# Kernel optimization log

Measured on AMD Instinct MI355X. Metric: run time of the kernel, lower is better.

The kernel has to match this reference:

```python
import jax, jax.numpy as jnp
import numpy as np

SEQ = 64      # len(features): number of timesteps for the (seq-major) LSTM
B = 40        # the expand(.., 40, ..) axis -> LSTM batch dim (batch_first=False)
IN = 8192 * 2 # 16384
H = 1024


def setup_inputs() -> dict:
    key = jax.random.key(0)
    k1, k2, k3, k4, k5 = jax.random.split(key, 5)
    s = 1.0 / np.sqrt(H)  # PyTorch LSTM init scale
    features = jax.random.normal(k1, (SEQ, IN), dtype=jnp.float32)
    w_ih = jax.random.uniform(k2, (4 * H, IN), jnp.float32, -s, s)
    w_hh = jax.random.uniform(k3, (4 * H, H), jnp.float32, -s, s)
    b_ih = jax.random.uniform(k4, (4 * H,), jnp.float32, -s, s)
    b_hh = jax.random.uniform(k5, (4 * H,), jnp.float32, -s, s)
    return {"features": features, "w_ih": w_ih, "w_hh": w_hh, "b_ih": b_ih, "b_hh": b_hh}


def reference(features, w_ih, w_hh, b_ih, b_hh):
    # features: [SEQ, IN]. The torch code expands each row to 40 identical
    # batch elements; since the input projection is identical across those
    # copies we compute it once per timestep and broadcast over B.
    xw = features @ w_ih.T + (b_ih + b_hh)  # [SEQ, 4H], hoisted big GEMM

    def step(carry, xw_t):
        h, c = carry                      # each [B, H]
        gates = xw_t[None, :] + h @ w_hh.T  # [B, 4H]
        i, f, g, o = jnp.split(gates, 4, axis=-1)  # PyTorch gate order i,f,g,o
        i = jax.nn.sigmoid(i)
        f = jax.nn.sigmoid(f)
        g = jnp.tanh(g)
        o = jax.nn.sigmoid(o)
        c = f * c + i * g
        h = o * jnp.tanh(c)
        return (h, c), h

    h0 = jnp.zeros((B, H), dtype=features.dtype)
    c0 = jnp.zeros((B, H), dtype=features.dtype)
    _, hs = jax.lax.scan(step, (h0, c0), xw)
    return hs  # [SEQ, B, H] == (seq_len, batch, hidden) as torch returns
```

## Files before the change

kernel.cpp:

```cpp
#include <hip/hip_runtime.h>
#include <hip/hip_bf16.h>
#include <math.h>

#define SEQ 64
#define IN_DIM 16384
#define H_DIM 1024
#define G4 4096
#define BATCH 40
#define NB_SCAN 64
#define NT_SCAN 1024

#define OFF_FT   256
#define OFF_XW   (OFF_FT + (size_t)IN_DIM*SEQ)
#define OFF_H    (OFF_XW + (size_t)SEQ*G4)
#define OFF_HS   (OFF_H + H_DIM)
#define OFF_PART (OFF_HS + (size_t)SEQ*H_DIM)

__global__ void zero_bar(unsigned* bar) {
    bar[threadIdx.x] = 0u;
}

__global__ __launch_bounds__(256) void transpose_f(const float* __restrict__ f,
                                                   float* __restrict__ fT) {
    __shared__ float lds[64][65];
    const int kb = blockIdx.x;
    const int tx = threadIdx.x & 63;
    const int ty = threadIdx.x >> 6;
#pragma unroll
    for (int i = 0; i < 16; ++i) {
        int t = ty * 16 + i;
        lds[tx][t] = f[(size_t)t * IN_DIM + kb * 64 + tx];
    }
    __syncthreads();
#pragma unroll
    for (int i = 0; i < 16; ++i) {
        int r = ty * 16 + i;
        fT[(size_t)(kb * 64 + r) * 64 + tx] = lds[r][tx];
    }
}

__global__ __launch_bounds__(256) void gemm_partial(const float* __restrict__ w_ih,
                                                    const float* __restrict__ fT,
                                                    float* __restrict__ part,
                                                    int kspan) {
    const int tid = threadIdx.x;
    const int j  = blockIdx.x * 256 + tid;
    const int t0 = blockIdx.y * 16;
    const int k0 = blockIdx.z * kspan;

    float acc[16];
#pragma unroll
    for (int i = 0; i < 16; ++i) acc[i] = 0.f;

    const float* wrow = w_ih + (size_t)j * IN_DIM;
    for (int kc = k0; kc < k0 + kspan; kc += 16) {
        const float4* wp = (const float4*)(wrow + kc);
        float warr[16];
        *(float4*)&warr[0]  = wp[0];
        *(float4*)&warr[4]  = wp[1];
        *(float4*)&warr[8]  = wp[2];
        *(float4*)&warr[12] = wp[3];
        const float* fbase = fT + (size_t)kc * 64 + t0;
#pragma unroll
        for (int kk = 0; kk < 16; ++kk) {
            const float wv = warr[kk];
            const float4* fp = (const float4*)(fbase + kk * 64);
            float4 f0 = fp[0], f1 = fp[1], f2 = fp[2], f3 = fp[3];
            acc[0]  += wv * f0.x; acc[1]  += wv * f0.y; acc[2]  += wv * f0.z; acc[3]  += wv * f0.w;
            acc[4]  += wv * f1.x; acc[5]  += wv * f1.y; acc[6]  += wv * f1.z; acc[7]  += wv * f1.w;
            acc[8]  += wv * f2.x; acc[9]  += wv * f2.y; acc[10] += wv * f2.z; acc[11] += wv * f2.w;
            acc[12] += wv * f3.x; acc[13] += wv * f3.y; acc[14] += wv * f3.z; acc[15] += wv * f3.w;
        }
    }
    float* pp = part + ((size_t)blockIdx.z * SEQ + t0) * G4 + j;
#pragma unroll
    for (int i = 0; i < 16; ++i) pp[(size_t)i * G4] = acc[i];
}

__global__ __launch_bounds__(256) void reduce_xw(const float* __restrict__ part,
                                                 const float* __restrict__ b_ih,
                                                 const float* __restrict__ b_hh,
                                                 float* __restrict__ xw, int KS) {
    const int idx = blockIdx.x * 256 + threadIdx.x;
    const int j = idx & (G4 - 1);
    float s = b_ih[j] + b_hh[j];
    for (int ks = 0; ks < KS; ++ks) s += part[(size_t)ks * (SEQ * G4) + idx];
    xw[idx] = s;
}

__global__ __launch_bounds__(NT_SCAN, 1) void lstm_scan(const float* __restrict__ xw,
                                                        const float* __restrict__ w_hh,
                                                        float* __restrict__ h_buf,
                                                        float* __restrict__ hs_c,
                                                        unsigned* __restrict__ bar) {
    const int tid = threadIdx.x;
    const int b = blockIdx.x;
    const int r  = tid & 63;
    const int q  = tid >> 6;
    const int g  = r >> 4;
    const int jl = r & 15;
    const size_t grow = (size_t)g * H_DIM + (size_t)b * 16 + jl;

    float4 w[16];
    {
        const float4* wp = (const float4*)(w_hh + grow * H_DIM + q * 64);
#pragma unroll
        for (int m = 0; m < 16; ++m) w[m] = wp[m];
    }
#pragma unroll
    for (int m = 0; m < 16; ++m) {
        asm volatile("" : "+v"(w[m].x), "+v"(w[m].y), "+v"(w[m].z), "+v"(w[m].w));
    }

    __shared__ float h_lds[H_DIM];
    __shared__ float red[64][17];
    __shared__ float gate_lds[64];

    float c_reg = 0.f;

    for (int t = 0; t < SEQ; ++t) {
        float part = 0.f;
        if (t > 0) {
            h_lds[tid] = __hip_atomic_load(h_buf + tid, __ATOMIC_RELAXED,
                                           __HIP_MEMORY_SCOPE_AGENT);
            __syncthreads();
#pragma unroll
            for (int m = 0; m < 16; ++m) {
                float4 h4 = *(const float4*)&h_lds[q * 64 + m * 4];
                part += w[m].x * h4.x + w[m].y * h4.y + w[m].z * h4.z + w[m].w * h4.w;
            }
        }
        red[r][q] = part;
        __syncthreads();
        if (tid < 64) {
            float s = 0.f;
#pragma unroll
            for (int qq = 0; qq < 16; ++qq) s += red[tid][qq];
            const int gg = tid >> 4;
            const int jj = b * 16 + (tid & 15);
            gate_lds[tid] = xw[(size_t)t * G4 + (size_t)gg * H_DIM + jj] + s;
        }
        __syncthreads();
        if (tid < 16) {
            float iv = gate_lds[tid];
            float fv = gate_lds[16 + tid];
            float gv = gate_lds[32 + tid];
            float ov = gate_lds[48 + tid];
            iv = 1.f / (1.f + expf(-iv));
            fv = 1.f / (1.f + expf(-fv));
            gv = tanhf(gv);
            ov = 1.f / (1.f + expf(-ov));
            c_reg = fv * c_reg + iv * gv;
            float hv = ov * tanhf(c_reg);
            const int j = b * 16 + tid;
            hs_c[(size_t)t * H_DIM + j] = hv;
            __hip_atomic_store(h_buf + j, hv, __ATOMIC_RELAXED,
                               __HIP_MEMORY_SCOPE_AGENT);
        }
        if (t < SEQ - 1) {
            __syncthreads();
            asm volatile("s_waitcnt vmcnt(0)" ::: "memory");
            if (tid == 0) {
                __hip_atomic_fetch_add(bar, 1u, __ATOMIC_RELAXED, __HIP_MEMORY_SCOPE_AGENT);
                const unsigned target = (unsigned)(NB_SCAN * (t + 1));
                while (__hip_atomic_load(bar, __ATOMIC_RELAXED, __HIP_MEMORY_SCOPE_AGENT) < target) {
                    __builtin_amdgcn_s_sleep(1);
                }
                asm volatile("" ::: "memory");
            }
            __syncthreads();
        }
    }
}

__global__ __launch_bounds__(256) void bcast_out(const float* __restrict__ hs_c,
                                                 float* __restrict__ out) {
    const int gi = blockIdx.x * 256 + threadIdx.x;
    const int t = gi / (BATCH * (H_DIM / 4));
    const int rem = gi - t * (BATCH * (H_DIM / 4));
    const int jq = rem & (H_DIM / 4 - 1);
    const float4 v = ((const float4*)hs_c)[t * (H_DIM / 4) + jq];
    ((float4*)out)[gi] = v;
}

extern "C" void kernel_launch(void* const* d_in, const int* in_sizes, int n_in,
                              void* d_out, int out_size, void* d_ws, size_t ws_size,
                              hipStream_t stream) {
    const float* features = (const float*)d_in[0];
    const float* w_ih     = (const float*)d_in[1];
    const float* w_hh     = (const float*)d_in[2];
    const float* b_ih     = (const float*)d_in[3];
    const float* b_hh     = (const float*)d_in[4];
    float* out = (float*)d_out;
    float* ws  = (float*)d_ws;

    float* fT    = ws + OFF_FT;
    float* xw    = ws + OFF_XW;
    float* h_buf = ws + OFF_H;
    float* hs_c  = ws + OFF_HS;
    float* part  = ws + OFF_PART;
    unsigned* bar = (unsigned*)d_ws;

    int KS = 16;
    while (KS > 1 && (OFF_PART + (size_t)KS * SEQ * G4) * 4 > ws_size) KS >>= 1;
    const int kspan = IN_DIM / KS;

    zero_bar<<<1, 256, 0, stream>>>(bar);
    transpose_f<<<IN_DIM / 64, 256, 0, stream>>>(features, fT);
    gemm_partial<<<dim3(G4 / 256, SEQ / 16, KS), 256, 0, stream>>>(w_ih, fT, part, kspan);
    reduce_xw<<<(SEQ * G4) / 256, 256, 0, stream>>>(part, b_ih, b_hh, xw, KS);
    lstm_scan<<<NB_SCAN, NT_SCAN, 0, stream>>>(xw, w_hh, h_buf, hs_c, bar);
    bcast_out<<<(SEQ * BATCH * H_DIM / 4) / 256, 256, 0, stream>>>(hs_c, out);
}
```

Baseline: 725.9 us.

## Use split-bf16 MFMA for input GEMM and per-block flag barrier in LSTM scan

Replaces the scalar FP32 input-projection GEMM with a bf16 MFMA kernel that splits both operands into hi/lo bf16 parts and uses three MFMAs to approximate FP32 precision. The feature transpose is replaced by a hi/lo conversion kernel, and the K-split count drops from 16 to 8. The LSTM scan drops the separate h buffer and reads h directly from the hs output, prefetches xw early in each step, and replaces the single atomic-counter barrier with per-block step flags polled by one wavefront. The split-bf16 approach drops the lo*lo term, adding a small precision loss, and weights are converted on the fly in every block.

```diff
diff --git a/kernel.cpp b/kernel.cpp
--- a/kernel.cpp
+++ b/kernel.cpp
@@ -10,71 +10,98 @@
 #define NB_SCAN 64
 #define NT_SCAN 1024
 
-#define OFF_FT   256
-#define OFF_XW   (OFF_FT + (size_t)IN_DIM*SEQ)
-#define OFF_H    (OFF_XW + (size_t)SEQ*G4)
-#define OFF_HS   (OFF_H + H_DIM)
-#define OFF_PART (OFF_HS + (size_t)SEQ*H_DIM)
-
-__global__ void zero_bar(unsigned* bar) {
-    bar[threadIdx.x] = 0u;
-}
-
-__global__ __launch_bounds__(256) void transpose_f(const float* __restrict__ f,
-                                                   float* __restrict__ fT) {
-    __shared__ float lds[64][65];
-    const int kb = blockIdx.x;
-    const int tx = threadIdx.x & 63;
-    const int ty = threadIdx.x >> 6;
-#pragma unroll
-    for (int i = 0; i < 16; ++i) {
-        int t = ty * 16 + i;
-        lds[tx][t] = f[(size_t)t * IN_DIM + kb * 64 + tx];
+typedef short bf16x8 __attribute__((ext_vector_type(8)));
+typedef float f32x4 __attribute__((ext_vector_type(4)));
+typedef unsigned int uvec4 __attribute__((ext_vector_type(4)));
+typedef unsigned int uvec2 __attribute__((ext_vector_type(2)));
+
+#define OFF_AH   256
+#define OFF_AL   (OFF_AH + (size_t)SEQ * IN_DIM / 2)
+#define OFF_XW   (OFF_AL + (size_t)SEQ * IN_DIM / 2)
+#define OFF_HS   (OFF_XW + (size_t)SEQ * G4)
+#define OFF_PART (OFF_HS + (size_t)SEQ * H_DIM)
+
+__global__ void zero_bar(unsigned* bar) { bar[threadIdx.x] = 0u; }
+
+__global__ __launch_bounds__(256) void convert_a(const float* __restrict__ f,
+                                                 unsigned* __restrict__ a_hi,
+                                                 unsigned* __restrict__ a_lo) {
+    const int i = blockIdx.x * 256 + threadIdx.x;
+    uvec4 u = ((const uvec4*)f)[i];
+    unsigned h0 = (u.x >> 16) | (u.y & 0xffff0000u);
+    unsigned h1 = (u.z >> 16) | (u.w & 0xffff0000u);
+    float l0 = __uint_as_float(u.x) - __uint_as_float(u.x & 0xffff0000u);
+    float l1 = __uint_as_float(u.y) - __uint_as_float(u.y & 0xffff0000u);
+    float l2 = __uint_as_float(u.z) - __uint_as_float(u.z & 0xffff0000u);
+    float l3 = __uint_as_float(u.w) - __uint_as_float(u.w & 0xffff0000u);
+    unsigned q0 = (__float_as_uint(l0) >> 16) | (__float_as_uint(l1) & 0xffff0000u);
+    unsigned q1 = (__float_as_uint(l2) >> 16) | (__float_as_uint(l3) & 0xffff0000u);
+    uvec2 hv; hv.x = h0; hv.y = h1;
+    uvec2 lv; lv.x = q0; lv.y = q1;
+    ((uvec2*)a_hi)[i] = hv;
+    ((uvec2*)a_lo)[i] = lv;
+}
+
+__global__ __launch_bounds__(256, 2) void gemm_mfma(const float* __restrict__ w_ih,
+                                                    const unsigned* __restrict__ a_hi,
+                                                    const unsigned* __restrict__ a_lo,
+                                                    float* __restrict__ part, int kspan) {
+    const int tid = threadIdx.x;
+    const int wv   = tid >> 6;
+    const int lane = tid & 63;
+    const int col  = lane & 15;
+    const int kg   = lane >> 4;
+    const int jbase = blockIdx.x * 64 + wv * 16 + col;
+    const int k0base = blockIdx.y * kspan;
+
+    const float* wrow = w_ih + (size_t)jbase * IN_DIM;
+
+    f32x4 acc[4] = {};
+
+    for (int k0 = k0base; k0 < k0base + kspan; k0 += 32) {
+        const int kf = k0 + kg * 8;
+        uvec4 u0 = *(const uvec4*)(wrow + kf);
+        uvec4 u1 = *(const uvec4*)(wrow + kf + 4);
+        uvec4 hb, lb;
+        hb.x = (u0.x >> 16) | (u0.y & 0xffff0000u);
+        hb.y = (u0.z >> 16) | (u0.w & 0xffff0000u);
+        hb.z = (u1.x >> 16) | (u1.y & 0xffff0000u);
+        hb.w = (u1.z >> 16) | (u1.w & 0xffff0000u);
+        float f0 = __uint_as_float(u0.x) - __uint_as_float(u0.x & 0xffff0000u);
+        float f1 = __uint_as_float(u0.y) - __uint_as_float(u0.y & 0xffff0000u);
+        float f2 = __uint_as_float(u0.z) - __uint_as_float(u0.z & 0xffff0000u);
+        float f3 = __uint_as_float(u0.w) - __uint_as_float(u0.w & 0xffff0000u);
+        float f4 = __uint_as_float(u1.x) - __uint_as_float(u1.x & 0xffff0000u);
+        float f5 = __uint_as_float(u1.y) - __uint_as_float(u1.y & 0xffff0000u);
+        float f6 = __uint_as_float(u1.z) - __uint_as_float(u1.z & 0xffff0000u);
+        float f7 = __uint_as_float(u1.w) - __uint_as_float(u1.w & 0xffff0000u);
+        lb.x = (__float_as_uint(f0) >> 16) | (__float_as_uint(f1) & 0xffff0000u);
+        lb.y = (__float_as_uint(f2) >> 16) | (__float_as_uint(f3) & 0xffff0000u);
+        lb.z = (__float_as_uint(f4) >> 16) | (__float_as_uint(f5) & 0xffff0000u);
+        lb.w = (__float_as_uint(f6) >> 16) | (__float_as_uint(f7) & 0xffff0000u);
+        bf16x8 bhi = __builtin_bit_cast(bf16x8, hb);
+        bf16x8 blo = __builtin_bit_cast(bf16x8, lb);
+
+#pragma unroll
+        for (int i = 0; i < 4; ++i) {
+            const size_t aidx = (size_t)(i * 16 + col) * (IN_DIM / 2) + (kf >> 1);
+            uvec4 ah = *(const uvec4*)(a_hi + aidx);
+            uvec4 al = *(const uvec4*)(a_lo + aidx);
+            bf16x8 ahv = __builtin_bit_cast(bf16x8, ah);
+            bf16x8 alv = __builtin_bit_cast(bf16x8, al);
+            acc[i] = __builtin_amdgcn_mfma_f32_16x16x32_bf16(ahv, bhi, acc[i], 0, 0, 0);
+            acc[i] = __builtin_amdgcn_mfma_f32_16x16x32_bf16(alv, bhi, acc[i], 0, 0, 0);
+            acc[i] = __builtin_amdgcn_mfma_f32_16x16x32_bf16(ahv, blo, acc[i], 0, 0, 0);
+        }
     }
-    __syncthreads();
-#pragma unroll
-    for (int i = 0; i < 16; ++i) {
-        int r = ty * 16 + i;
-        fT[(size_t)(kb * 64 + r) * 64 + tx] = lds[r][tx];
-    }
-}
-
-__global__ __launch_bounds__(256) void gemm_partial(const float* __restrict__ w_ih,
-                                                    const float* __restrict__ fT,
-                                                    float* __restrict__ part,
-                                                    int kspan) {
-    const int tid = threadIdx.x;
-    const int j  = blockIdx.x * 256 + tid;
-    const int t0 = blockIdx.y * 16;
-    const int k0 = blockIdx.z * kspan;
-
-    float acc[16];
-#pragma unroll
-    for (int i = 0; i < 16; ++i) acc[i] = 0.f;
-
-    const float* wrow = w_ih + (size_t)j * IN_DIM;
-    for (int kc = k0; kc < k0 + kspan; kc += 16) {
-        const float4* wp = (const float4*)(wrow + kc);
-        float warr[16];
-        *(float4*)&warr[0]  = wp[0];
-        *(float4*)&warr[4]  = wp[1];
-        *(float4*)&warr[8]  = wp[2];
-        *(float4*)&warr[12] = wp[3];
-        const float* fbase = fT + (size_t)kc * 64 + t0;
-#pragma unroll
-        for (int kk = 0; kk < 16; ++kk) {
-            const float wv = warr[kk];
-            const float4* fp = (const float4*)(fbase + kk * 64);
-            float4 f0 = fp[0], f1 = fp[1], f2 = fp[2], f3 = fp[3];
-            acc[0]  += wv * f0.x; acc[1]  += wv * f0.y; acc[2]  += wv * f0.z; acc[3]  += wv * f0.w;
-            acc[4]  += wv * f1.x; acc[5]  += wv * f1.y; acc[6]  += wv * f1.z; acc[7]  += wv * f1.w;
-            acc[8]  += wv * f2.x; acc[9]  += wv * f2.y; acc[10] += wv * f2.z; acc[11] += wv * f2.w;
-            acc[12] += wv * f3.x; acc[13] += wv * f3.y; acc[14] += wv * f3.z; acc[15] += wv * f3.w;
-        }
-    }
-    float* pp = part + ((size_t)blockIdx.z * SEQ + t0) * G4 + j;
-#pragma unroll
-    for (int i = 0; i < 16; ++i) pp[(size_t)i * G4] = acc[i];
+    float* pb = part + (size_t)blockIdx.y * (SEQ * G4);
+#pragma unroll
+    for (int i = 0; i < 4; ++i)
+#pragma unroll
+        for (int r = 0; r < 4; ++r) {
+            const int trow = i * 16 + kg * 4 + r;
+            pb[(size_t)trow * G4 + jbase] = acc[i][r];
+        }
 }
 
 __global__ __launch_bounds__(256) void reduce_xw(const float* __restrict__ part,
@@ -90,14 +117,13 @@
 
 __global__ __launch_bounds__(NT_SCAN, 1) void lstm_scan(const float* __restrict__ xw,
                                                         const float* __restrict__ w_hh,
-                                                        float* __restrict__ h_buf,
                                                         float* __restrict__ hs_c,
                                                         unsigned* __restrict__ bar) {
     const int tid = threadIdx.x;
     const int b = blockIdx.x;
-    const int r  = tid & 63;
-    const int q  = tid >> 6;
-    const int g  = r >> 4;
+    const int r = tid & 63;
+    const int q = tid >> 6;
+    const int g = r >> 4;
     const int jl = r & 15;
     const size_t grow = (size_t)g * H_DIM + (size_t)b * 16 + jl;
 
@@ -108,9 +134,8 @@
         for (int m = 0; m < 16; ++m) w[m] = wp[m];
     }
 #pragma unroll
-    for (int m = 0; m < 16; ++m) {
+    for (int m = 0; m < 16; ++m)
         asm volatile("" : "+v"(w[m].x), "+v"(w[m].y), "+v"(w[m].z), "+v"(w[m].w));
-    }
 
     __shared__ float h_lds[H_DIM];
     __shared__ float red[64][17];
@@ -119,26 +144,27 @@
     float c_reg = 0.f;
 
     for (int t = 0; t < SEQ; ++t) {
-        float part = 0.f;
+        float xwv = 0.f;
+        if (tid < 64)
+            xwv = xw[(size_t)t * G4 + (size_t)(tid >> 4) * H_DIM + b * 16 + (tid & 15)];
+        float acc = 0.f;
         if (t > 0) {
-            h_lds[tid] = __hip_atomic_load(h_buf + tid, __ATOMIC_RELAXED,
-                                           __HIP_MEMORY_SCOPE_AGENT);
+            h_lds[tid] = __hip_atomic_load(hs_c + (size_t)(t - 1) * H_DIM + tid,
+                                           __ATOMIC_RELAXED, __HIP_MEMORY_SCOPE_AGENT);
             __syncthreads();
 #pragma unroll
             for (int m = 0; m < 16; ++m) {
                 float4 h4 = *(const float4*)&h_lds[q * 64 + m * 4];
-                part += w[m].x * h4.x + w[m].y * h4.y + w[m].z * h4.z + w[m].w * h4.w;
+                acc += w[m].x * h4.x + w[m].y * h4.y + w[m].z * h4.z + w[m].w * h4.w;
             }
         }
-        red[r][q] = part;
+        red[r][q] = acc;
         __syncthreads();
         if (tid < 64) {
             float s = 0.f;
 #pragma unroll
             for (int qq = 0; qq < 16; ++qq) s += red[tid][qq];
-            const int gg = tid >> 4;
-            const int jj = b * 16 + (tid & 15);
-            gate_lds[tid] = xw[(size_t)t * G4 + (size_t)gg * H_DIM + jj] + s;
+            gate_lds[tid] = xwv + s;
         }
         __syncthreads();
         if (tid < 16) {
@@ -152,19 +178,22 @@
             ov = 1.f / (1.f + expf(-ov));
             c_reg = fv * c_reg + iv * gv;
             float hv = ov * tanhf(c_reg);
-            const int j = b * 16 + tid;
-            hs_c[(size_t)t * H_DIM + j] = hv;
-            __hip_atomic_store(h_buf + j, hv, __ATOMIC_RELAXED,
-                               __HIP_MEMORY_SCOPE_AGENT);
+            __hip_atomic_store(hs_c + (size_t)t * H_DIM + b * 16 + tid, hv,
+                               __ATOMIC_RELAXED, __HIP_MEMORY_SCOPE_AGENT);
         }
         if (t < SEQ - 1) {
-            __syncthreads();
             asm volatile("s_waitcnt vmcnt(0)" ::: "memory");
-            if (tid == 0) {
-                __hip_atomic_fetch_add(bar, 1u, __ATOMIC_RELAXED, __HIP_MEMORY_SCOPE_AGENT);
-                const unsigned target = (unsigned)(NB_SCAN * (t + 1));
-                while (__hip_atomic_load(bar, __ATOMIC_RELAXED, __HIP_MEMORY_SCOPE_AGENT) < target) {
+            if (tid == 0)
+                __hip_atomic_store(bar + b, (unsigned)t + 1u,
+                                   __ATOMIC_RELAXED, __HIP_MEMORY_SCOPE_AGENT);
+            if (tid < 64) {
+                const unsigned target = (unsigned)t + 1u;
+                unsigned v = __hip_atomic_load(bar + tid, __ATOMIC_RELAXED,
+                                               __HIP_MEMORY_SCOPE_AGENT);
+                while (__all((int)(v >= target)) == 0) {
                     __builtin_amdgcn_s_sleep(1);
+                    v = __hip_atomic_load(bar + tid, __ATOMIC_RELAXED,
+                                          __HIP_MEMORY_SCOPE_AGENT);
                 }
                 asm volatile("" ::: "memory");
             }
@@ -194,21 +223,21 @@
     float* out = (float*)d_out;
     float* ws  = (float*)d_ws;
 
-    float* fT    = ws + OFF_FT;
-    float* xw    = ws + OFF_XW;
-    float* h_buf = ws + OFF_H;
-    float* hs_c  = ws + OFF_HS;
-    float* part  = ws + OFF_PART;
-    unsigned* bar = (unsigned*)d_ws;
-
-    int KS = 16;
+    unsigned* bar  = (unsigned*)d_ws;
+    unsigned* a_hi = (unsigned*)(ws + OFF_AH);
+    unsigned* a_lo = (unsigned*)(ws + OFF_AL);
+    float* xw   = ws + OFF_XW;
+    float* hs_c = ws + OFF_HS;
+    float* part = ws + OFF_PART;
+
+    int KS = 8;
     while (KS > 1 && (OFF_PART + (size_t)KS * SEQ * G4) * 4 > ws_size) KS >>= 1;
     const int kspan = IN_DIM / KS;
 
     zero_bar<<<1, 256, 0, stream>>>(bar);
-    transpose_f<<<IN_DIM / 64, 256, 0, stream>>>(features, fT);
-    gemm_partial<<<dim3(G4 / 256, SEQ / 16, KS), 256, 0, stream>>>(w_ih, fT, part, kspan);
+    convert_a<<<(SEQ * IN_DIM / 4) / 256, 256, 0, stream>>>(features, a_hi, a_lo);
+    gemm_mfma<<<dim3(G4 / 64, KS), 256, 0, stream>>>(w_ih, a_hi, a_lo, part, kspan);
     reduce_xw<<<(SEQ * G4) / 256, 256, 0, stream>>>(part, b_ih, b_hh, xw, KS);
-    lstm_scan<<<NB_SCAN, NT_SCAN, 0, stream>>>(xw, w_hh, h_buf, hs_c, bar);
+    lstm_scan<<<NB_SCAN, NT_SCAN, 0, stream>>>(xw, w_hh, hs_c, bar);
     bcast_out<<<(SEQ * BATCH * H_DIM / 4) / 256, 256, 0, stream>>>(hs_c, out);
 }
```

Result: no change. 738.6 us (+1.7%).
